# Optimization experiments

Hardware: AMD Instinct MI355X
Metric: run time of the kernel (lower is better)

## Reference

```python
import jax, jax.numpy as jnp
import numpy as np

N, B, T, D = 4, 4, 512, 512
H, DK, DV = 8, 64, 64
LN_EPS = 1e-5


def setup_inputs() -> dict:
    key = jax.random.key(0)
    ks = jax.random.split(key, 5)
    s = 1.0 / np.sqrt(D)
    return {
        "x": jax.random.normal(ks[0], (N, B, T, D), jnp.float32),
        "Wq": jax.random.normal(ks[1], (D, H * DK), jnp.float32) * s,
        "bq": jnp.zeros((H * DK,), jnp.float32),
        "Wk": jax.random.normal(ks[2], (D, H * DK), jnp.float32) * s,
        "bk": jnp.zeros((H * DK,), jnp.float32),
        "Wv": jax.random.normal(ks[3], (D, H * DV), jnp.float32) * s,
        "bv": jnp.zeros((H * DV,), jnp.float32),
        "Wo": jax.random.normal(ks[4], (H * DV, D), jnp.float32) * (1.0 / np.sqrt(H * DV)),
        "bo": jnp.zeros((D,), jnp.float32),
        "gamma": jnp.ones((D,), jnp.float32),
        "beta": jnp.zeros((D,), jnp.float32),
    }


def reference(x, Wq, bq, Wk, bk, Wv, bv, Wo, bo, gamma, beta):
    # x: [N, B, T, D] -- N variables, each [B, T, D]
    n = x.shape[0]
    # Project once per variable (the torch code redundantly recomputes K/V per query var).
    q = (x @ Wq + bq).reshape(n, B, T, H, DK).transpose(0, 1, 3, 2, 4)  # [N,B,H,T,DK]
    k = (x @ Wk + bk).reshape(n, B, T, H, DK).transpose(0, 1, 3, 2, 4)  # [N,B,H,T,DK]
    v = (x @ Wv + bv).reshape(n, B, T, H, DV).transpose(0, 1, 3, 2, 4)  # [N,B,H,T,DV]
    # All-pairs attention: softmax over keys of EACH key-variable separately.
    scores = jnp.einsum('qbhtk,cbhsk->qcbhts', q, k) / np.sqrt(DK)  # [Nq,Nc,B,H,T,T]
    attn = jax.nn.softmax(scores, axis=-1)
    ctx = jnp.einsum('qcbhts,cbhsv->qcbhtv', attn, v)  # [Nq,Nc,B,H,T,DV]
    ctx = ctx.transpose(0, 1, 2, 4, 3, 5).reshape(n, n, B, T, H * DV)
    out = ctx @ Wo + bo                     # per-pair output projection
    out = out.sum(axis=1) / n               # average over key variables -> [N,B,T,D]
    res = x + out
    mu = res.mean(axis=-1, keepdims=True)
    var = res.var(axis=-1, keepdims=True)
    y = (res - mu) / jnp.sqrt(var + LN_EPS) * gamma + beta
    return y
```

## Files before the change

kernel.cpp:

```cpp
#include <hip/hip_runtime.h>


typedef __bf16 bf16x8 __attribute__((ext_vector_type(8)));
typedef __bf16 bf16x4 __attribute__((ext_vector_type(4)));
typedef short shortx4 __attribute__((ext_vector_type(4)));
typedef float floatx4 __attribute__((ext_vector_type(4)));
typedef float floatx16 __attribute__((ext_vector_type(16)));
typedef unsigned short ushortx8 __attribute__((ext_vector_type(8)));

static __device__ __forceinline__ unsigned short f2bf(float f) {
  union { __bf16 h; unsigned short u; } c; c.h = (__bf16)f; return c.u;
}
static __device__ __forceinline__ float bf2f(unsigned short u) {
  union { unsigned u32; float f; } c; c.u32 = ((unsigned)u) << 16; return c.f;
}

#define QSCALE 0.18033688011112042f
#define SHIFT2 (-17.312340489609306f)

__global__ __launch_bounds__(256) void prep(
    const float* __restrict__ Wq, const float* __restrict__ Wk,
    const float* __restrict__ Wv, const float* __restrict__ Wo,
    const float* __restrict__ x,
    unsigned short* __restrict__ wqkvT, unsigned short* __restrict__ woT,
    unsigned short* __restrict__ x_bf)
{
  const int bid = blockIdx.x;
  const int tid = threadIdx.x;
  if (bid < 256) {
    __shared__ unsigned short lds[64][65];
    const int z = bid >> 6, rest = bid & 63;
    const int k0 = (rest >> 3) * 64, n0 = (rest & 7) * 64;
    const float* W; unsigned short* T;
    if (z == 0)      { W = Wq; T = wqkvT; }
    else if (z == 1) { W = Wk; T = wqkvT + 262144; }
    else if (z == 2) { W = Wv; T = wqkvT + 524288; }
    else             { W = Wo; T = woT; }
    const int xx = tid & 63, yy = tid >> 6;
#pragma unroll
    for (int i = 0; i < 16; ++i) {
      const int row = yy * 16 + i;
      lds[row][xx] = f2bf(W[(size_t)(k0 + row) * 512 + n0 + xx]);
    }
    __syncthreads();
#pragma unroll
    for (int i = 0; i < 16; ++i) {
      const int nr = yy * 16 + i;
      T[(size_t)(n0 + nr) * 512 + k0 + xx] = lds[xx][nr];
    }
  } else {
    const int i = (bid - 256) * 256 + tid;
    const float4 a = ((const float4*)x)[i * 2];
    const float4 b = ((const float4*)x)[i * 2 + 1];
    ushortx8 o;
    o[0] = f2bf(a.x); o[1] = f2bf(a.y); o[2] = f2bf(a.z); o[3] = f2bf(a.w);
    o[4] = f2bf(b.x); o[5] = f2bf(b.y); o[6] = f2bf(b.z); o[7] = f2bf(b.w);
    *(ushortx8*)(x_bf + (size_t)i * 8) = o;
  }
}

__global__ __launch_bounds__(256) void gemm_qkv(
    const unsigned short* __restrict__ Xb,
    const unsigned short* __restrict__ BT,
    const float* __restrict__ bq, const float* __restrict__ bk,
    const float* __restrict__ bv,
    unsigned short* __restrict__ Qo, unsigned short* __restrict__ Ko,
    unsigned short* __restrict__ Vo)
{
  __shared__ __align__(16) unsigned short lA[128][72];
  __shared__ __align__(16) unsigned short lB[128][72];
  const int tid  = threadIdx.x;
  const int wv   = tid >> 6, lane = tid & 63;
  const int quad = lane >> 4, l16 = lane & 15;
  const int wm = wv >> 1, wn = wv & 1;
  const int m0  = blockIdx.x * 128;
  const int by  = blockIdx.y;
  const int n0g = by * 128;
  const int sel = by >> 2;
  const float* bias = (sel == 0) ? bq : (sel == 1) ? bk : bv;
  const float scale = (sel == 0) ? QSCALE : 1.0f;
  unsigned short* outp = (sel == 0) ? Qo : (sel == 1) ? Ko : Vo;

  floatx4 acc[4][4] = {};
  const int srow = tid >> 1, sc0 = (tid & 1) * 32;

  for (int kc = 0; kc < 512; kc += 64) {
    __syncthreads();
    const unsigned short* as = Xb + (size_t)(m0 + srow) * 512 + kc + sc0;
    const unsigned short* bs = BT + (size_t)(n0g + srow) * 512 + kc + sc0;
#pragma unroll
    for (int j = 0; j < 4; ++j) {
      *(bf16x8*)&lA[srow][sc0 + j * 8] = *(const bf16x8*)(as + j * 8);
      *(bf16x8*)&lB[srow][sc0 + j * 8] = *(const bf16x8*)(bs + j * 8);
    }
    __syncthreads();
    bf16x8 af[4][2];
#pragma unroll
    for (int ti = 0; ti < 4; ++ti) {
      af[ti][0] = *(const bf16x8*)&lA[wm * 64 + ti * 16 + l16][quad * 8];
      af[ti][1] = *(const bf16x8*)&lA[wm * 64 + ti * 16 + l16][32 + quad * 8];
    }
#pragma unroll
    for (int ni = 0; ni < 4; ++ni) {
      bf16x8 b0 = *(const bf16x8*)&lB[wn * 64 + ni * 16 + l16][quad * 8];
      bf16x8 b1 = *(const bf16x8*)&lB[wn * 64 + ni * 16 + l16][32 + quad * 8];
#pragma unroll
      for (int ti = 0; ti < 4; ++ti) {
        acc[ti][ni] = __builtin_amdgcn_mfma_f32_16x16x32_bf16(af[ti][0], b0, acc[ti][ni], 0, 0, 0);
        acc[ti][ni] = __builtin_amdgcn_mfma_f32_16x16x32_bf16(af[ti][1], b1, acc[ti][ni], 0, 0, 0);
      }
    }
  }

#pragma unroll
  for (int ni = 0; ni < 4; ++ni) {
    const int n = (n0g & 511) + wn * 64 + ni * 16 + l16;
    const float bvv = bias[n];
    const int hh = n >> 6, dk = n & 63;
#pragma unroll
    for (int ti = 0; ti < 4; ++ti) {
      const int mb = m0 + wm * 64 + ti * 16 + quad * 4;
#pragma unroll
      for (int r = 0; r < 4; ++r) {
        const int m = mb + r;
        const int nb = m >> 9, t = m & 511;
        const float v = (acc[ti][ni][r] + bvv) * scale;
        if (sel == 2)
          outp[((size_t)(nb * 8 + hh) * 64 + dk) * 512 + t] = f2bf(v);
        else
          outp[((size_t)(nb * 8 + hh) * 512 + t) * 64 + dk] = f2bf(v);
      }
    }
  }
}

__global__ __launch_bounds__(256) void gemm_out(
    const unsigned short* __restrict__ C0, const unsigned short* __restrict__ C1,
    const unsigned short* __restrict__ BT, float* __restrict__ Cout)
{
  __shared__ __align__(16) unsigned short lA[128][72];
  __shared__ __align__(16) unsigned short lB[128][72];
  const int tid  = threadIdx.x;
  const int wv   = tid >> 6, lane = tid & 63;
  const int quad = lane >> 4, l16 = lane & 15;
  const int wm = wv >> 1, wn = wv & 1;
  const int m0 = blockIdx.x * 128, n0 = blockIdx.y * 128;

  floatx4 acc[4][4] = {};
  const int srow = tid >> 1, sc0 = (tid & 1) * 32;

  for (int kc = 0; kc < 512; kc += 64) {
    __syncthreads();
    const size_t aoff = (size_t)(m0 + srow) * 512 + kc + sc0;
    const unsigned short* bs = BT + (size_t)(n0 + srow) * 512 + kc + sc0;
#pragma unroll
    for (int j = 0; j < 4; ++j) {
      ushortx8 a0 = *(const ushortx8*)(C0 + aoff + j * 8);
      ushortx8 a1 = *(const ushortx8*)(C1 + aoff + j * 8);
      ushortx8 o;
#pragma unroll
      for (int e = 0; e < 8; ++e) o[e] = f2bf(bf2f(a0[e]) + bf2f(a1[e]));
      *(ushortx8*)&lA[srow][sc0 + j * 8] = o;
      *(bf16x8*)&lB[srow][sc0 + j * 8] = *(const bf16x8*)(bs + j * 8);
    }
    __syncthreads();
    bf16x8 af[4][2];
#pragma unroll
    for (int ti = 0; ti < 4; ++ti) {
      af[ti][0] = *(const bf16x8*)&lA[wm * 64 + ti * 16 + l16][quad * 8];
      af[ti][1] = *(const bf16x8*)&lA[wm * 64 + ti * 16 + l16][32 + quad * 8];
    }
#pragma unroll
    for (int ni = 0; ni < 4; ++ni) {
      bf16x8 b0 = *(const bf16x8*)&lB[wn * 64 + ni * 16 + l16][quad * 8];
      bf16x8 b1 = *(const bf16x8*)&lB[wn * 64 + ni * 16 + l16][32 + quad * 8];
#pragma unroll
      for (int ti = 0; ti < 4; ++ti) {
        acc[ti][ni] = __builtin_amdgcn_mfma_f32_16x16x32_bf16(af[ti][0], b0, acc[ti][ni], 0, 0, 0);
        acc[ti][ni] = __builtin_amdgcn_mfma_f32_16x16x32_bf16(af[ti][1], b1, acc[ti][ni], 0, 0, 0);
      }
    }
  }

#pragma unroll
  for (int ni = 0; ni < 4; ++ni) {
    const int n = n0 + wn * 64 + ni * 16 + l16;
#pragma unroll
    for (int ti = 0; ti < 4; ++ti) {
      const int mb = m0 + wm * 64 + ti * 16 + quad * 4;
#pragma unroll
      for (int r = 0; r < 4; ++r)
        Cout[(size_t)(mb + r) * 512 + n] = acc[ti][ni][r];
    }
  }
}

__global__ __launch_bounds__(256) void flash_kernel(
    const unsigned short* __restrict__ Q,
    const unsigned short* __restrict__ K,
    const unsigned short* __restrict__ VT,
    unsigned short* __restrict__ CTX2)
{
  __shared__ __align__(16) unsigned short lK[2][64][72];
  __shared__ __align__(16) unsigned short lV[2][64][68];
  const int tid  = threadIdx.x;
  const int wv   = tid >> 6, lane = tid & 63;
  const int l32  = lane & 31, u = lane >> 5;

  const int lin  = blockIdx.x;
  const int xcd  = lin & 7, slot = lin >> 3;
  const int tile = slot & 3;
  const int nbh  = xcd * 16 + ((slot >> 2) & 15);
  const int cg   = slot >> 6;
  const int t0   = tile * 128;
  const int h = nbh & 7, nb = nbh >> 3, b = nb & 3;

  const unsigned short* qbase = Q + ((size_t)nbh * 512 + (t0 + wv * 32 + l32)) * 64;
  bf16x8 qf[4];
#pragma unroll
  for (int c16 = 0; c16 < 4; ++c16)
    qf[c16] = *(const bf16x8*)(qbase + c16 * 16 + u * 8);

  const int srow = tid >> 2, sc0 = (tid & 3) * 16;
  const unsigned short *kptr, *vptr;
  auto setptr = [&](int it) {
    const int c = cg * 2 + (it >> 3), s0 = (it & 7) * 64;
    const size_t kvbh = (size_t)((c * 4 + b) * 8 + h);
    kptr = K  + kvbh * (512 * 64) + (size_t)(s0 + srow) * 64 + sc0;
    vptr = VT + kvbh * (64 * 512) + (size_t)srow * 512 + s0 + sc0;
  };
  bf16x8 rk0, rk1, rv0, rv1;
  auto loadregs = [&]() {
    rk0 = *(const bf16x8*)kptr; rk1 = *(const bf16x8*)(kptr + 8);
    rv0 = *(const bf16x8*)vptr; rv1 = *(const bf16x8*)(vptr + 8);
  };
  auto writebuf = [&](int p) {
    *(bf16x8*)&lK[p][srow][sc0]     = rk0;
    *(bf16x8*)&lK[p][srow][sc0 + 8] = rk1;
    union { bf16x8 v8; bf16x4 v4[2]; } c0, c1;
    c0.v8 = rv0; c1.v8 = rv1;
    *(bf16x4*)&lV[p][srow][sc0]      = c0.v4[0];
    *(bf16x4*)&lV[p][srow][sc0 + 4]  = c0.v4[1];
    *(bf16x4*)&lV[p][srow][sc0 + 8]  = c1.v4[0];
    *(bf16x4*)&lV[p][srow][sc0 + 12] = c1.v4[1];
  };

  setptr(0); loadregs();
  writebuf(0);
  setptr(1); loadregs();
  __syncthreads();

  floatx16 ofin0 = {}, ofin1 = {};
  floatx16 oc0, oc1;
  float lacc;

  for (int it = 0; it < 16; ++it) {
    const int cur = it & 1;
    const int st = it & 7;
    if (st == 0) { oc0 = floatx16{}; oc1 = floatx16{}; lacc = 0.f; }

    if (it < 15) writebuf(cur ^ 1);
    if (it < 14) { setptr(it + 2); loadregs(); }

    floatx16 sacc0, sacc1;
#pragma unroll
    for (int r = 0; r < 16; ++r) { sacc0[r] = SHIFT2; sacc1[r] = SHIFT2; }
#pragma unroll
    for (int c16 = 0; c16 < 4; ++c16) {
      bf16x8 ak0 = *(const bf16x8*)&lK[cur][l32][c16 * 16 + u * 8];
      bf16x8 ak1 = *(const bf16x8*)&lK[cur][32 + l32][c16 * 16 + u * 8];
      sacc0 = __builtin_amdgcn_mfma_f32_32x32x16_bf16(ak0, qf[c16], sacc0, 0, 0, 0);
      sacc1 = __builtin_amdgcn_mfma_f32_32x32x16_bf16(ak1, qf[c16], sacc1, 0, 0, 0);
    }

#pragma unroll
    for (int sb = 0; sb < 2; ++sb) {
      const floatx16& sa = sb ? sacc1 : sacc0;
#pragma unroll
      for (int c8 = 0; c8 < 4; ++c8) {
        float e0 = __builtin_amdgcn_exp2f(sa[4 * c8 + 0]);
        float e1 = __builtin_amdgcn_exp2f(sa[4 * c8 + 1]);
        float e2 = __builtin_amdgcn_exp2f(sa[4 * c8 + 2]);
        float e3 = __builtin_amdgcn_exp2f(sa[4 * c8 + 3]);
        lacc += (e0 + e1) + (e2 + e3);
        shortx4 pf;
        pf[0] = (short)f2bf(e0); pf[1] = (short)f2bf(e1);
        pf[2] = (short)f2bf(e2); pf[3] = (short)f2bf(e3);
        const int sloc = sb * 32 + c8 * 8 + u * 4;
        shortx4 vf0 = *(const shortx4*)&lV[cur][l32][sloc];
        shortx4 vf1 = *(const shortx4*)&lV[cur][32 + l32][sloc];
        oc0 = __builtin_amdgcn_mfma_f32_32x32x8bf16_1k(pf, vf0, oc0, 0, 0, 0);
        oc1 = __builtin_amdgcn_mfma_f32_32x32x8bf16_1k(pf, vf1, oc1, 0, 0, 0);
      }
    }

    if (st == 7) {
      float s = lacc;
      s += __shfl_xor(s, 32);
      const float inv = 1.0f / s;
#pragma unroll
      for (int r = 0; r < 16; ++r) {
        const int trow = (r & 3) + 8 * (r >> 2) + 4 * u;
        const float invr = __shfl(inv, trow);
        ofin0[r] += oc0[r] * invr;
        ofin1[r] += oc1[r] * invr;
      }
    }
    __syncthreads();
  }

  unsigned short* outp = CTX2 + (size_t)cg * (8192 * 512);
  const int mbase = nb * 512 + t0 + wv * 32;
#pragma unroll
  for (int r = 0; r < 16; ++r) {
    const int trow = (r & 3) + 8 * (r >> 2) + 4 * u;
    const size_t rowoff = (size_t)(mbase + trow) * 512 + h * 64;
    outp[rowoff + l32]      = f2bf(ofin0[r]);
    outp[rowoff + 32 + l32] = f2bf(ofin1[r]);
  }
}

__global__ __launch_bounds__(256) void ln_kernel(
    const float* __restrict__ x, const float* __restrict__ tmp,
    const float* __restrict__ bo, const float* __restrict__ gamma,
    const float* __restrict__ beta, float* __restrict__ out)
{
  const int row = blockIdx.x;
  const int t = threadIdx.x;
  const size_t base = (size_t)row * 512;
  const float r0 = x[base + t]       + 0.25f * tmp[base + t]       + bo[t];
  const float r1 = x[base + t + 256] + 0.25f * tmp[base + t + 256] + bo[t + 256];
  float s = r0 + r1, sq = r0 * r0 + r1 * r1;
#pragma unroll
  for (int off = 1; off < 64; off <<= 1) {
    s  += __shfl_xor(s, off);
    sq += __shfl_xor(sq, off);
  }
  __shared__ float ls[4], lq[4];
  const int wv = t >> 6, lane = t & 63;
  if (lane == 0) { ls[wv] = s; lq[wv] = sq; }
  __syncthreads();
  s  = ls[0] + ls[1] + ls[2] + ls[3];
  sq = lq[0] + lq[1] + lq[2] + lq[3];
  const float mu  = s * (1.0f / 512.0f);
  const float var = sq * (1.0f / 512.0f) - mu * mu;
  const float inv = rsqrtf(var + 1e-5f);
  out[base + t]       = (r0 - mu) * inv * gamma[t]       + beta[t];
  out[base + t + 256] = (r1 - mu) * inv * gamma[t + 256] + beta[t + 256];
}

extern "C" void kernel_launch(void* const* d_in, const int* in_sizes, int n_in,
                              void* d_out, int out_size, void* d_ws, size_t ws_size,
                              hipStream_t stream) {
  const float* x     = (const float*)d_in[0];
  const float* Wq    = (const float*)d_in[1];
  const float* bq    = (const float*)d_in[2];
  const float* Wk    = (const float*)d_in[3];
  const float* bk    = (const float*)d_in[4];
  const float* Wv    = (const float*)d_in[5];
  const float* bv    = (const float*)d_in[6];
  const float* Wo    = (const float*)d_in[7];
  const float* bo    = (const float*)d_in[8];
  const float* gamma = (const float*)d_in[9];
  const float* beta  = (const float*)d_in[10];
  float* out = (float*)d_out;

  char* w = (char*)d_ws;
  unsigned short* q_bf  = (unsigned short*)(w);
  unsigned short* k_bf  = (unsigned short*)(w + (size_t)8  * 1024 * 1024);
  unsigned short* vt_bf = (unsigned short*)(w + (size_t)16 * 1024 * 1024);
  unsigned short* x_bf  = (unsigned short*)(w + (size_t)24 * 1024 * 1024);
  unsigned short* ctx2  = (unsigned short*)(w + (size_t)24 * 1024 * 1024);
  unsigned short* wqkvT = (unsigned short*)(w + (size_t)40 * 1024 * 1024);
  unsigned short* woT   = wqkvT + 786432;
  float* tmp            = (float*)(w);

  prep<<<2304, 256, 0, stream>>>(Wq, Wk, Wv, Wo, x, wqkvT, woT, x_bf);
  gemm_qkv<<<dim3(64, 12), 256, 0, stream>>>(x_bf, wqkvT, bq, bk, bv,
                                             q_bf, k_bf, vt_bf);
  flash_kernel<<<1024, 256, 0, stream>>>(q_bf, k_bf, vt_bf, ctx2);
  gemm_out<<<dim3(64, 4), 256, 0, stream>>>(ctx2, ctx2 + (size_t)8192 * 512,
                                            woT, tmp);
  ln_kernel<<<8192, 256, 0, stream>>>(x, tmp, bo, gamma, beta, out);
}
```

Measured before the change: 197.6 us.

## Split flash attention per key-variable with fp32 atomic accumulation, fuse x cast into QKV GEMM

Each flash block now handles a single key variable instead of two, which doubles the grid to 2048 blocks and halves the per-block loop. Per-variable normalized contexts are summed with fp32 atomicAdd into a buffer that prep zero-fills, and gemm_out converts that buffer to bf16 on load. The separate x-to-bf16 pre-pass is removed because gemm_qkv now converts fp32 x while staging it, and its grid axes are swapped. LayerNorm is rewritten to use one wave per row with float4 accesses and no LDS reduction. The costs are atomic contention, fp32 context traffic at twice the size, and the extra zero-fill writes.

```diff
diff --git a/kernel.cpp b/kernel.cpp
--- a/kernel.cpp
+++ b/kernel.cpp
@@ -11,9 +11,6 @@
 static __device__ __forceinline__ unsigned short f2bf(float f) {
   union { __bf16 h; unsigned short u; } c; c.h = (__bf16)f; return c.u;
 }
-static __device__ __forceinline__ float bf2f(unsigned short u) {
-  union { unsigned u32; float f; } c; c.u32 = ((unsigned)u) << 16; return c.f;
-}
 
 #define QSCALE 0.18033688011112042f
 #define SHIFT2 (-17.312340489609306f)
@@ -21,9 +18,8 @@
 __global__ __launch_bounds__(256) void prep(
     const float* __restrict__ Wq, const float* __restrict__ Wk,
     const float* __restrict__ Wv, const float* __restrict__ Wo,
-    const float* __restrict__ x,
     unsigned short* __restrict__ wqkvT, unsigned short* __restrict__ woT,
-    unsigned short* __restrict__ x_bf)
+    float* __restrict__ ctxf)
 {
   const int bid = blockIdx.x;
   const int tid = threadIdx.x;
@@ -49,18 +45,14 @@
       T[(size_t)(n0 + nr) * 512 + k0 + xx] = lds[xx][nr];
     }
   } else {
-    const int i = (bid - 256) * 256 + tid;
-    const float4 a = ((const float4*)x)[i * 2];
-    const float4 b = ((const float4*)x)[i * 2 + 1];
-    ushortx8 o;
-    o[0] = f2bf(a.x); o[1] = f2bf(a.y); o[2] = f2bf(a.z); o[3] = f2bf(a.w);
-    o[4] = f2bf(b.x); o[5] = f2bf(b.y); o[6] = f2bf(b.z); o[7] = f2bf(b.w);
-    *(ushortx8*)(x_bf + (size_t)i * 8) = o;
+    const size_t i = ((size_t)(bid - 256) * 256 + tid) * 8;
+    *(float4*)(ctxf + i)     = float4{0.f, 0.f, 0.f, 0.f};
+    *(float4*)(ctxf + i + 4) = float4{0.f, 0.f, 0.f, 0.f};
   }
 }
 
 __global__ __launch_bounds__(256) void gemm_qkv(
-    const unsigned short* __restrict__ Xb,
+    const float* __restrict__ X,
     const unsigned short* __restrict__ BT,
     const float* __restrict__ bq, const float* __restrict__ bk,
     const float* __restrict__ bv,
@@ -73,10 +65,9 @@
   const int wv   = tid >> 6, lane = tid & 63;
   const int quad = lane >> 4, l16 = lane & 15;
   const int wm = wv >> 1, wn = wv & 1;
-  const int m0  = blockIdx.x * 128;
-  const int by  = blockIdx.y;
-  const int n0g = by * 128;
-  const int sel = by >> 2;
+  const int n0g = blockIdx.x * 128;
+  const int m0  = blockIdx.y * 128;
+  const int sel = n0g >> 9;
   const float* bias = (sel == 0) ? bq : (sel == 1) ? bk : bv;
   const float scale = (sel == 0) ? QSCALE : 1.0f;
   unsigned short* outp = (sel == 0) ? Qo : (sel == 1) ? Ko : Vo;
@@ -86,11 +77,16 @@
 
   for (int kc = 0; kc < 512; kc += 64) {
     __syncthreads();
-    const unsigned short* as = Xb + (size_t)(m0 + srow) * 512 + kc + sc0;
+    const float* as = X + (size_t)(m0 + srow) * 512 + kc + sc0;
     const unsigned short* bs = BT + (size_t)(n0g + srow) * 512 + kc + sc0;
 #pragma unroll
     for (int j = 0; j < 4; ++j) {
-      *(bf16x8*)&lA[srow][sc0 + j * 8] = *(const bf16x8*)(as + j * 8);
+      float4 f0 = *(const float4*)(as + j * 8);
+      float4 f1 = *(const float4*)(as + j * 8 + 4);
+      ushortx8 p;
+      p[0]=f2bf(f0.x); p[1]=f2bf(f0.y); p[2]=f2bf(f0.z); p[3]=f2bf(f0.w);
+      p[4]=f2bf(f1.x); p[5]=f2bf(f1.y); p[6]=f2bf(f1.z); p[7]=f2bf(f1.w);
+      *(ushortx8*)&lA[srow][sc0 + j * 8] = p;
       *(bf16x8*)&lB[srow][sc0 + j * 8] = *(const bf16x8*)(bs + j * 8);
     }
     __syncthreads();
@@ -135,8 +131,8 @@
 }
 
 __global__ __launch_bounds__(256) void gemm_out(
-    const unsigned short* __restrict__ C0, const unsigned short* __restrict__ C1,
-    const unsigned short* __restrict__ BT, float* __restrict__ Cout)
+    const float* __restrict__ Cf, const unsigned short* __restrict__ BT,
+    float* __restrict__ Cout)
 {
   __shared__ __align__(16) unsigned short lA[128][72];
   __shared__ __align__(16) unsigned short lB[128][72];
@@ -151,16 +147,16 @@
 
   for (int kc = 0; kc < 512; kc += 64) {
     __syncthreads();
-    const size_t aoff = (size_t)(m0 + srow) * 512 + kc + sc0;
+    const float* as = Cf + (size_t)(m0 + srow) * 512 + kc + sc0;
     const unsigned short* bs = BT + (size_t)(n0 + srow) * 512 + kc + sc0;
 #pragma unroll
     for (int j = 0; j < 4; ++j) {
-      ushortx8 a0 = *(const ushortx8*)(C0 + aoff + j * 8);
-      ushortx8 a1 = *(const ushortx8*)(C1 + aoff + j * 8);
-      ushortx8 o;
-#pragma unroll
-      for (int e = 0; e < 8; ++e) o[e] = f2bf(bf2f(a0[e]) + bf2f(a1[e]));
-      *(ushortx8*)&lA[srow][sc0 + j * 8] = o;
+      float4 f0 = *(const float4*)(as + j * 8);
+      float4 f1 = *(const float4*)(as + j * 8 + 4);
+      ushortx8 p;
+      p[0]=f2bf(f0.x); p[1]=f2bf(f0.y); p[2]=f2bf(f0.z); p[3]=f2bf(f0.w);
+      p[4]=f2bf(f1.x); p[5]=f2bf(f1.y); p[6]=f2bf(f1.z); p[7]=f2bf(f1.w);
+      *(ushortx8*)&lA[srow][sc0 + j * 8] = p;
       *(bf16x8*)&lB[srow][sc0 + j * 8] = *(const bf16x8*)(bs + j * 8);
     }
     __syncthreads();
@@ -199,7 +195,7 @@
     const unsigned short* __restrict__ Q,
     const unsigned short* __restrict__ K,
     const unsigned short* __restrict__ VT,
-    unsigned short* __restrict__ CTX2)
+    float* __restrict__ CTXF)
 {
   __shared__ __align__(16) unsigned short lK[2][64][72];
   __shared__ __align__(16) unsigned short lV[2][64][68];
@@ -211,7 +207,7 @@
   const int xcd  = lin & 7, slot = lin >> 3;
   const int tile = slot & 3;
   const int nbh  = xcd * 16 + ((slot >> 2) & 15);
-  const int cg   = slot >> 6;
+  const int c    = slot >> 6;
   const int t0   = tile * 128;
   const int h = nbh & 7, nb = nbh >> 3, b = nb & 3;
 
@@ -220,14 +216,17 @@
 #pragma unroll
   for (int c16 = 0; c16 < 4; ++c16)
     qf[c16] = *(const bf16x8*)(qbase + c16 * 16 + u * 8);
+
+  const size_t kvbh = (size_t)((c * 4 + b) * 8 + h);
+  const unsigned short* kb = K  + kvbh * (512 * 64);
+  const unsigned short* vb = VT + kvbh * (64 * 512);
 
   const int srow = tid >> 2, sc0 = (tid & 3) * 16;
   const unsigned short *kptr, *vptr;
   auto setptr = [&](int it) {
-    const int c = cg * 2 + (it >> 3), s0 = (it & 7) * 64;
-    const size_t kvbh = (size_t)((c * 4 + b) * 8 + h);
-    kptr = K  + kvbh * (512 * 64) + (size_t)(s0 + srow) * 64 + sc0;
-    vptr = VT + kvbh * (64 * 512) + (size_t)srow * 512 + s0 + sc0;
+    const int s0 = it * 64;
+    kptr = kb + (size_t)(s0 + srow) * 64 + sc0;
+    vptr = vb + (size_t)srow * 512 + s0 + sc0;
   };
   bf16x8 rk0, rk1, rv0, rv1;
   auto loadregs = [&]() {
@@ -250,17 +249,14 @@
   setptr(1); loadregs();
   __syncthreads();
 
-  floatx16 ofin0 = {}, ofin1 = {};
-  floatx16 oc0, oc1;
-  float lacc;
-
-  for (int it = 0; it < 16; ++it) {
+  floatx16 oc0 = {}, oc1 = {};
+  float lacc = 0.f;
+
+  for (int it = 0; it < 8; ++it) {
     const int cur = it & 1;
-    const int st = it & 7;
-    if (st == 0) { oc0 = floatx16{}; oc1 = floatx16{}; lacc = 0.f; }
-
-    if (it < 15) writebuf(cur ^ 1);
-    if (it < 14) { setptr(it + 2); loadregs(); }
+
+    if (it < 7) writebuf(cur ^ 1);
+    if (it < 6) { setptr(it + 2); loadregs(); }
 
     floatx16 sacc0, sacc1;
 #pragma unroll
@@ -293,30 +289,20 @@
         oc1 = __builtin_amdgcn_mfma_f32_32x32x8bf16_1k(pf, vf1, oc1, 0, 0, 0);
       }
     }
-
-    if (st == 7) {
-      float s = lacc;
-      s += __shfl_xor(s, 32);
-      const float inv = 1.0f / s;
-#pragma unroll
-      for (int r = 0; r < 16; ++r) {
-        const int trow = (r & 3) + 8 * (r >> 2) + 4 * u;
-        const float invr = __shfl(inv, trow);
-        ofin0[r] += oc0[r] * invr;
-        ofin1[r] += oc1[r] * invr;
-      }
-    }
-    __syncthreads();
-  }
-
-  unsigned short* outp = CTX2 + (size_t)cg * (8192 * 512);
+    __syncthreads();
+  }
+
+  float s = lacc;
+  s += __shfl_xor(s, 32);
+  const float inv = 1.0f / s;
   const int mbase = nb * 512 + t0 + wv * 32;
 #pragma unroll
   for (int r = 0; r < 16; ++r) {
     const int trow = (r & 3) + 8 * (r >> 2) + 4 * u;
+    const float invr = __shfl(inv, trow);
     const size_t rowoff = (size_t)(mbase + trow) * 512 + h * 64;
-    outp[rowoff + l32]      = f2bf(ofin0[r]);
-    outp[rowoff + 32 + l32] = f2bf(ofin1[r]);
+    atomicAdd(&CTXF[rowoff + l32],      oc0[r] * invr);
+    atomicAdd(&CTXF[rowoff + 32 + l32], oc1[r] * invr);
   }
 }
 
@@ -325,28 +311,43 @@
     const float* __restrict__ bo, const float* __restrict__ gamma,
     const float* __restrict__ beta, float* __restrict__ out)
 {
-  const int row = blockIdx.x;
-  const int t = threadIdx.x;
-  const size_t base = (size_t)row * 512;
-  const float r0 = x[base + t]       + 0.25f * tmp[base + t]       + bo[t];
-  const float r1 = x[base + t + 256] + 0.25f * tmp[base + t + 256] + bo[t + 256];
-  float s = r0 + r1, sq = r0 * r0 + r1 * r1;
+  const int wv   = threadIdx.x >> 6, lane = threadIdx.x & 63;
+  const int row  = blockIdx.x * 4 + wv;
+  const int col  = lane * 8;
+  const size_t base = (size_t)row * 512 + col;
+  const float4 x0 = *(const float4*)(x + base);
+  const float4 x1 = *(const float4*)(x + base + 4);
+  const float4 t0 = *(const float4*)(tmp + base);
+  const float4 t1 = *(const float4*)(tmp + base + 4);
+  const float4 b0 = *(const float4*)(bo + col);
+  const float4 b1 = *(const float4*)(bo + col + 4);
+  float r[8];
+  r[0] = x0.x + 0.25f * t0.x + b0.x;  r[1] = x0.y + 0.25f * t0.y + b0.y;
+  r[2] = x0.z + 0.25f * t0.z + b0.z;  r[3] = x0.w + 0.25f * t0.w + b0.w;
+  r[4] = x1.x + 0.25f * t1.x + b1.x;  r[5] = x1.y + 0.25f * t1.y + b1.y;
+  r[6] = x1.z + 0.25f * t1.z + b1.z;  r[7] = x1.w + 0.25f * t1.w + b1.w;
+  float s = 0.f, sq = 0.f;
+#pragma unroll
+  for (int j = 0; j < 8; ++j) { s += r[j]; sq += r[j] * r[j]; }
 #pragma unroll
   for (int off = 1; off < 64; off <<= 1) {
     s  += __shfl_xor(s, off);
     sq += __shfl_xor(sq, off);
   }
-  __shared__ float ls[4], lq[4];
-  const int wv = t >> 6, lane = t & 63;
-  if (lane == 0) { ls[wv] = s; lq[wv] = sq; }
-  __syncthreads();
-  s  = ls[0] + ls[1] + ls[2] + ls[3];
-  sq = lq[0] + lq[1] + lq[2] + lq[3];
   const float mu  = s * (1.0f / 512.0f);
   const float var = sq * (1.0f / 512.0f) - mu * mu;
   const float inv = rsqrtf(var + 1e-5f);
-  out[base + t]       = (r0 - mu) * inv * gamma[t]       + beta[t];
-  out[base + t + 256] = (r1 - mu) * inv * gamma[t + 256] + beta[t + 256];
+  const float4 g0 = *(const float4*)(gamma + col);
+  const float4 g1 = *(const float4*)(gamma + col + 4);
+  const float4 be0 = *(const float4*)(beta + col);
+  const float4 be1 = *(const float4*)(beta + col + 4);
+  float4 o0, o1;
+  o0.x = (r[0] - mu) * inv * g0.x + be0.x;  o0.y = (r[1] - mu) * inv * g0.y + be0.y;
+  o0.z = (r[2] - mu) * inv * g0.z + be0.z;  o0.w = (r[3] - mu) * inv * g0.w + be0.w;
+  o1.x = (r[4] - mu) * inv * g1.x + be1.x;  o1.y = (r[5] - mu) * inv * g1.y + be1.y;
+  o1.z = (r[6] - mu) * inv * g1.z + be1.z;  o1.w = (r[7] - mu) * inv * g1.w + be1.w;
+  *(float4*)(out + base)     = o0;
+  *(float4*)(out + base + 4) = o1;
 }
 
 extern "C" void kernel_launch(void* const* d_in, const int* in_sizes, int n_in,
@@ -369,17 +370,15 @@
   unsigned short* q_bf  = (unsigned short*)(w);
   unsigned short* k_bf  = (unsigned short*)(w + (size_t)8  * 1024 * 1024);
   unsigned short* vt_bf = (unsigned short*)(w + (size_t)16 * 1024 * 1024);
-  unsigned short* x_bf  = (unsigned short*)(w + (size_t)24 * 1024 * 1024);
-  unsigned short* ctx2  = (unsigned short*)(w + (size_t)24 * 1024 * 1024);
+  float* ctxf           = (float*)(w + (size_t)24 * 1024 * 1024);
   unsigned short* wqkvT = (unsigned short*)(w + (size_t)40 * 1024 * 1024);
   unsigned short* woT   = wqkvT + 786432;
   float* tmp            = (float*)(w);
 
-  prep<<<2304, 256, 0, stream>>>(Wq, Wk, Wv, Wo, x, wqkvT, woT, x_bf);
-  gemm_qkv<<<dim3(64, 12), 256, 0, stream>>>(x_bf, wqkvT, bq, bk, bv,
+  prep<<<2304, 256, 0, stream>>>(Wq, Wk, Wv, Wo, wqkvT, woT, ctxf);
+  gemm_qkv<<<dim3(12, 64), 256, 0, stream>>>(x, wqkvT, bq, bk, bv,
                                              q_bf, k_bf, vt_bf);
-  flash_kernel<<<1024, 256, 0, stream>>>(q_bf, k_bf, vt_bf, ctx2);
-  gemm_out<<<dim3(64, 4), 256, 0, stream>>>(ctx2, ctx2 + (size_t)8192 * 512,
-                                            woT, tmp);
-  ln_kernel<<<8192, 256, 0, stream>>>(x, tmp, bo, gamma, beta, out);
-}
+  flash_kernel<<<2048, 256, 0, stream>>>(q_bf, k_bf, vt_bf, ctxf);
+  gemm_out<<<dim3(64, 4), 256, 0, stream>>>(ctxf, woT, tmp);
+  ln_kernel<<<2048, 256, 0, stream>>>(x, tmp, bo, gamma, beta, out);
+}
```

Measured after the change: 227.6 us. +15.2%, slower.
